# Performance work log

Hardware: AMD Instinct MI355X
Metric: run time of the kernel (lower is better)

The kernel has to match this reference:

```python
import jax, jax.numpy as jnp
import numpy as np


def setup_inputs() -> dict:
    key = jax.random.key(0)
    k1, k2, k3 = jax.random.split(key, 3)
    B, c_in, T, N = 16, 64, 64, 512
    K, c_out = 3, 64
    x = jax.random.normal(k1, (B, c_in, T, N), dtype=jnp.float32)
    # scaled Laplacian-like matrix; scale to keep Chebyshev recurrence stable
    La = jax.random.normal(k2, (B, N, N), dtype=jnp.float32) / jnp.sqrt(jnp.float32(N))
    # Conv2d(K*c_in, c_out, 1x1, bias=False) weight, squeezed to [c_out, K*c_in]
    W = jax.random.normal(k3, (c_out, K * c_in), dtype=jnp.float32) * 0.05
    return {"x": x, "La": La, "W": W}


def reference(x, La, W):
    # x: [B, c_in, T, N], La: [B, N, N], W: [c_out, K*c_in]
    B, c_in, T, N = x.shape
    K = W.shape[1] // c_in
    xp = jnp.transpose(x, (0, 1, 3, 2))  # [B, c_in, N, T] -> 'bcnl'
    # Chebyshev polynomial recurrence: T0 = I, T1 = La, Tk = 2*La@T_{k-1} - T_{k-2}
    I = jnp.broadcast_to(jnp.eye(N, dtype=x.dtype), (B, N, N))
    Ls = [I, La]
    L0, L1 = I, La
    for _ in range(2, K):
        L2 = 2.0 * jnp.matmul(La, L1) - L0
        L0, L1 = L1, L2
        Ls.append(L2)
    Lap = jnp.stack(Ls, axis=1)            # [B, K, N, N]
    Lap = jnp.swapaxes(Lap, -1, -2)        # transpose(-1,-2) as in torch
    # graph conv: contract over source node n
    y = jnp.einsum('bcnl,bknq->bckql', xp, Lap)  # [B, c_in, K, N, T]
    y = y.reshape(B, c_in * K, N, T)       # channel index = c*K + k
    # 1x1 conv, no bias: [c_out, c_in*K] x [B, c_in*K, N, T]
    out = jnp.einsum('oi,binl->bonl', W, y)  # [B, c_out, N, T]
    out = jnp.transpose(out, (0, 1, 3, 2))   # [B, c_out, T, N]
    return out
```

## Files before the change

kernel.cpp:

```cpp
#include <hip/hip_runtime.h>
#include <hip/hip_bf16.h>


#define B_   16
#define CIN  64
#define T_   64
#define N_   512
#define M_   4096
#define KDIM 512
#define COUT 64

typedef __bf16 bf16x8 __attribute__((ext_vector_type(8)));
typedef float  floatx4 __attribute__((ext_vector_type(4)));

__device__ __forceinline__ float bf2f(unsigned short u) {
    unsigned int v = ((unsigned int)u) << 16;
    return __builtin_bit_cast(float, v);
}
__device__ __forceinline__ unsigned short f2bf(float f) {
    unsigned int u = __builtin_bit_cast(unsigned int, f);
    unsigned int lsb = (u >> 16) & 1u;
    u += 0x7fffu + lsb;
    return (unsigned short)(u >> 16);
}

#define GLOAD_LDS16(gp, lp)                                                  \
    __builtin_amdgcn_global_load_lds(                                        \
        (const __attribute__((address_space(1))) void*)(gp),                 \
        (__attribute__((address_space(3))) void*)(lp), 16, 0, 0)

__global__ __launch_bounds__(256) void cvt_f32_bf16(
    const float* __restrict__ src, unsigned short* __restrict__ dst, int n)
{
    int i = (blockIdx.x * 256 + threadIdx.x) * 8;
    if (i + 8 <= n) {
        float4 a = *(const float4*)(src + i);
        float4 b = *(const float4*)(src + i + 4);
        union { unsigned short s[8]; uint4 u; } o;
        o.s[0] = f2bf(a.x); o.s[1] = f2bf(a.y); o.s[2] = f2bf(a.z); o.s[3] = f2bf(a.w);
        o.s[4] = f2bf(b.x); o.s[5] = f2bf(b.y); o.s[6] = f2bf(b.z); o.s[7] = f2bf(b.w);
        *(uint4*)(dst + i) = o.u;
    }
}

__global__ __launch_bounds__(256) void pack_w(
    const float* __restrict__ W, unsigned short* __restrict__ Wb)
{
    int idx = threadIdx.x + blockIdx.x * 256;
    if (idx < 64 * 192) {
        int o = idx / 192, j = idx % 192;
        int c = j & 63, k = j >> 6;
        Wb[idx] = f2bf(W[o * 192 + c * 3 + k]);
    }
}

#define BM 128
#define BN 128
#define BK 32

__global__ __launch_bounds__(256) void gemm_bt(
    const unsigned short* __restrict__ A,
    const unsigned short* __restrict__ Bm,
    unsigned short* __restrict__ C,
    const unsigned short* __restrict__ X,
    int mode)
{
    int batch = blockIdx.z;
    A  += (size_t)batch * M_ * KDIM;
    Bm += (size_t)batch * N_ * KDIM;
    C  += (size_t)batch * M_ * N_;
    X  += (size_t)batch * M_ * N_;
    int m0 = blockIdx.y * BM;
    int n0 = blockIdx.x * BN;

    __shared__ __align__(16) unsigned short As[BM * BK];
    __shared__ __align__(16) unsigned short Bs[BN * BK];

    int tid  = threadIdx.x;
    int lane = tid & 63;
    int wave = tid >> 6;
    int wm   = (wave >> 1) * 64;
    int wn   = (wave & 1) * 64;
    int l15  = lane & 15;
    int quad = lane >> 4;

    int r16 = lane >> 2;
    int sch = lane & 3;
    int gch = sch ^ (r16 & 3);

    const unsigned short* gA0 = A  + (size_t)(m0 + wave * 16 + r16) * KDIM + gch * 8;
    const unsigned short* gA1 = gA0 + (size_t)64 * KDIM;
    const unsigned short* gB0 = Bm + (size_t)(n0 + wave * 16 + r16) * KDIM + gch * 8;
    const unsigned short* gB1 = gB0 + (size_t)64 * KDIM;
    const unsigned short* lA0 = &As[(wave * 16) * BK];
    const unsigned short* lA1 = &As[(64 + wave * 16) * BK];
    const unsigned short* lB0 = &Bs[(wave * 16) * BK];
    const unsigned short* lB1 = &Bs[(64 + wave * 16) * BK];

    const uint4* afp[4];
    const uint4* bfp[4];
    int sl = quad ^ (l15 & 3);
#pragma unroll
    for (int im = 0; im < 4; im++)
        afp[im] = (const uint4*)((const char*)As + (wm + im * 16 + l15) * (BK * 2) + sl * 16);
#pragma unroll
    for (int jn = 0; jn < 4; jn++)
        bfp[jn] = (const uint4*)((const char*)Bs + (wn + jn * 16 + l15) * (BK * 2) + sl * 16);

    floatx4 acc[4][4];
#pragma unroll
    for (int i = 0; i < 4; i++)
#pragma unroll
        for (int j = 0; j < 4; j++) acc[i][j] = (floatx4)0.0f;

    for (int k0 = 0; k0 < KDIM; k0 += BK) {
        __syncthreads();
        GLOAD_LDS16(gA0 + k0, lA0);
        GLOAD_LDS16(gA1 + k0, lA1);
        GLOAD_LDS16(gB0 + k0, lB0);
        GLOAD_LDS16(gB1 + k0, lB1);
        __syncthreads();

        bf16x8 af[4], bf[4];
#pragma unroll
        for (int im = 0; im < 4; im++) af[im] = __builtin_bit_cast(bf16x8, *afp[im]);
#pragma unroll
        for (int jn = 0; jn < 4; jn++) bf[jn] = __builtin_bit_cast(bf16x8, *bfp[jn]);
#pragma unroll
        for (int im = 0; im < 4; im++)
#pragma unroll
            for (int jn = 0; jn < 4; jn++)
                acc[im][jn] = __builtin_amdgcn_mfma_f32_16x16x32_bf16(
                    af[im], bf[jn], acc[im][jn], 0, 0, 0);
    }

#pragma unroll
    for (int im = 0; im < 4; im++)
#pragma unroll
        for (int jn = 0; jn < 4; jn++) {
            int c = n0 + wn + jn * 16 + l15;
#pragma unroll
            for (int r = 0; r < 4; r++) {
                int m = m0 + wm + im * 16 + quad * 4 + r;
                size_t idx = (size_t)m * N_ + c;
                float v = acc[im][jn][r];
                if (mode) v = 2.0f * v - bf2f(X[idx]);
                C[idx] = f2bf(v);
            }
        }
}

#define PJ_PITCH 40

__global__ __launch_bounds__(256) void proj(
    const unsigned short* __restrict__ xb,
    const unsigned short* __restrict__ z1b,
    const unsigned short* __restrict__ z2b,
    const unsigned short* __restrict__ Wb,
    float* __restrict__ out)
{
    __shared__ __align__(16) unsigned short Ds[256 * PJ_PITCH];

    int b  = blockIdx.y;
    int n0 = blockIdx.x * 256;
    int tid  = threadIdx.x;
    int lane = tid & 63;
    int wave = tid >> 6;
    int l15  = lane & 15;
    int quad = lane >> 4;

    size_t boff = (size_t)b * M_ * N_ + n0;
    const unsigned short* zp[3] = { xb + boff, z1b + boff, z2b + boff };

    bf16x8 wf[6];
#pragma unroll
    for (int kc = 0; kc < 6; kc++)
        wf[kc] = __builtin_bit_cast(bf16x8,
            *(const uint4*)(Wb + (size_t)(wave * 16 + l15) * 192 + kc * 32 + quad * 8));

    floatx4 acc[16];
#pragma unroll
    for (int i = 0; i < 16; i++) acc[i] = (floatx4)0.0f;

    int jl  = tid & 31;
    int nc0 = (tid >> 5) * 8;

    for (int kc = 0; kc < 6; kc++) {
        const unsigned short* src =
            zp[kc >> 1] + (size_t)((kc & 1) * 32 + jl) * (T_ * N_) + nc0;
        uint4 v[4];
#pragma unroll
        for (int u = 0; u < 4; u++) v[u] = *(const uint4*)(src + u * 64);

        __syncthreads();
#pragma unroll
        for (int u = 0; u < 4; u++) {
            unsigned short* d = &Ds[(size_t)(nc0 + u * 64) * PJ_PITCH + jl];
            unsigned int w0 = v[u].x, w1 = v[u].y, w2 = v[u].z, w3 = v[u].w;
            d[0 * PJ_PITCH] = (unsigned short)w0;
            d[1 * PJ_PITCH] = (unsigned short)(w0 >> 16);
            d[2 * PJ_PITCH] = (unsigned short)w1;
            d[3 * PJ_PITCH] = (unsigned short)(w1 >> 16);
            d[4 * PJ_PITCH] = (unsigned short)w2;
            d[5 * PJ_PITCH] = (unsigned short)(w2 >> 16);
            d[6 * PJ_PITCH] = (unsigned short)w3;
            d[7 * PJ_PITCH] = (unsigned short)(w3 >> 16);
        }
        __syncthreads();

#pragma unroll
        for (int nt = 0; nt < 16; nt++) {
            bf16x8 bf = __builtin_bit_cast(bf16x8,
                *(const uint4*)(&Ds[(size_t)(nt * 16 + l15) * PJ_PITCH + quad * 8]));
            acc[nt] = __builtin_amdgcn_mfma_f32_16x16x32_bf16(wf[kc], bf, acc[nt], 0, 0, 0);
        }
    }

    float* ob = out + (size_t)b * COUT * (T_ * N_);
#pragma unroll
    for (int nt = 0; nt < 16; nt++) {
        int n = n0 + nt * 16 + l15;
#pragma unroll
        for (int r = 0; r < 4; r++) {
            int o = wave * 16 + quad * 4 + r;
            ob[(size_t)o * (T_ * N_) + n] = acc[nt][r];
        }
    }
}

extern "C" void kernel_launch(void* const* d_in, const int* in_sizes, int n_in,
                              void* d_out, int out_size, void* d_ws, size_t ws_size,
                              hipStream_t stream) {
    const float* x  = (const float*)d_in[0];
    const float* La = (const float*)d_in[1];
    const float* W  = (const float*)d_in[2];
    float* out = (float*)d_out;

    const size_t n_x  = (size_t)B_ * CIN * T_ * N_;
    const size_t n_La = (size_t)B_ * N_ * N_;

    char* ws = (char*)d_ws;
    unsigned short* xb  = (unsigned short*)ws;
    unsigned short* Lab = (unsigned short*)(ws + n_x * 2);
    unsigned short* z1b = (unsigned short*)(ws + n_x * 2 + n_La * 2);
    unsigned short* z2b = (unsigned short*)(ws + n_x * 4 + n_La * 2);
    unsigned short* Wb  = (unsigned short*)(ws + n_x * 6 + n_La * 2);

    cvt_f32_bf16<<<(int)(n_x / 2048),  256, 0, stream>>>(x,  xb,  (int)n_x);
    cvt_f32_bf16<<<(int)(n_La / 2048), 256, 0, stream>>>(La, Lab, (int)n_La);
    pack_w<<<48, 256, 0, stream>>>(W, Wb);

    dim3 gg(N_ / BN, M_ / BM, B_);
    gemm_bt<<<gg, 256, 0, stream>>>(xb,  Lab, z1b, xb, 0);
    gemm_bt<<<gg, 256, 0, stream>>>(z1b, Lab, z2b, xb, 1);

    dim3 gp((T_ * N_) / 256, B_);
    proj<<<gp, 256, 0, stream>>>(xb, z1b, z2b, Wb, out);
}
```

Baseline: 469.2 us.

## Triple-buffer GEMM LDS staging and rework projection transpose with perm-packed swizzled stores

```diff
diff --git a/kernel.cpp b/kernel.cpp
--- a/kernel.cpp
+++ b/kernel.cpp
@@ -12,6 +12,7 @@
 
 typedef __bf16 bf16x8 __attribute__((ext_vector_type(8)));
 typedef float  floatx4 __attribute__((ext_vector_type(4)));
+typedef unsigned int uintx4 __attribute__((ext_vector_type(4)));
 
 __device__ __forceinline__ float bf2f(unsigned short u) {
     unsigned int v = ((unsigned int)u) << 16;
@@ -57,6 +58,8 @@
 #define BM 128
 #define BN 128
 #define BK 32
+#define KIT  (KDIM / BK)
+#define SBUF (BM * BK)
 
 __global__ __launch_bounds__(256) void gemm_bt(
     const unsigned short* __restrict__ A,
@@ -73,8 +76,8 @@
     int m0 = blockIdx.y * BM;
     int n0 = blockIdx.x * BN;
 
-    __shared__ __align__(16) unsigned short As[BM * BK];
-    __shared__ __align__(16) unsigned short Bs[BN * BK];
+    __shared__ __align__(16) unsigned short As[3 * SBUF];
+    __shared__ __align__(16) unsigned short Bs[3 * SBUF];
 
     int tid  = threadIdx.x;
     int lane = tid & 63;
@@ -92,20 +95,27 @@
     const unsigned short* gA1 = gA0 + (size_t)64 * KDIM;
     const unsigned short* gB0 = Bm + (size_t)(n0 + wave * 16 + r16) * KDIM + gch * 8;
     const unsigned short* gB1 = gB0 + (size_t)64 * KDIM;
-    const unsigned short* lA0 = &As[(wave * 16) * BK];
-    const unsigned short* lA1 = &As[(64 + wave * 16) * BK];
-    const unsigned short* lB0 = &Bs[(wave * 16) * BK];
-    const unsigned short* lB1 = &Bs[(64 + wave * 16) * BK];
-
-    const uint4* afp[4];
-    const uint4* bfp[4];
+
+    int dA0 = (wave * 16) * BK;
+    int dA1 = (64 + wave * 16) * BK;
+    int dB0 = dA0;
+    int dB1 = dA1;
+
+#define STAGE(kk, bo) do {                                        \
+        GLOAD_LDS16(gA0 + (kk) * BK, &As[(bo) + dA0]);            \
+        GLOAD_LDS16(gA1 + (kk) * BK, &As[(bo) + dA1]);            \
+        GLOAD_LDS16(gB0 + (kk) * BK, &Bs[(bo) + dB0]);            \
+        GLOAD_LDS16(gB1 + (kk) * BK, &Bs[(bo) + dB1]);            \
+    } while (0)
+
+    int aoff[4], boff[4];
     int sl = quad ^ (l15 & 3);
 #pragma unroll
     for (int im = 0; im < 4; im++)
-        afp[im] = (const uint4*)((const char*)As + (wm + im * 16 + l15) * (BK * 2) + sl * 16);
+        aoff[im] = (wm + im * 16 + l15) * BK + sl * 8;
 #pragma unroll
     for (int jn = 0; jn < 4; jn++)
-        bfp[jn] = (const uint4*)((const char*)Bs + (wn + jn * 16 + l15) * (BK * 2) + sl * 16);
+        boff[jn] = (wn + jn * 16 + l15) * BK + sl * 8;
 
     floatx4 acc[4][4];
 #pragma unroll
@@ -113,19 +123,25 @@
 #pragma unroll
         for (int j = 0; j < 4; j++) acc[i][j] = (floatx4)0.0f;
 
-    for (int k0 = 0; k0 < KDIM; k0 += BK) {
-        __syncthreads();
-        GLOAD_LDS16(gA0 + k0, lA0);
-        GLOAD_LDS16(gA1 + k0, lA1);
-        GLOAD_LDS16(gB0 + k0, lB0);
-        GLOAD_LDS16(gB1 + k0, lB1);
-        __syncthreads();
-
+    STAGE(0, 0);
+    STAGE(1, SBUF);
+
+#pragma unroll
+    for (int k = 0; k < KIT; ++k) {
+        if (k < KIT - 1) asm volatile("s_waitcnt vmcnt(4)" ::: "memory");
+        else             asm volatile("s_waitcnt vmcnt(0)" ::: "memory");
+        __builtin_amdgcn_s_barrier();
+
+        if (k + 2 < KIT) STAGE(k + 2, ((k + 2) % 3) * SBUF);
+
+        const int cb = (k % 3) * SBUF;
         bf16x8 af[4], bf[4];
 #pragma unroll
-        for (int im = 0; im < 4; im++) af[im] = __builtin_bit_cast(bf16x8, *afp[im]);
-#pragma unroll
-        for (int jn = 0; jn < 4; jn++) bf[jn] = __builtin_bit_cast(bf16x8, *bfp[jn]);
+        for (int im = 0; im < 4; im++)
+            af[im] = __builtin_bit_cast(bf16x8, *(const uint4*)&As[cb + aoff[im]]);
+#pragma unroll
+        for (int jn = 0; jn < 4; jn++)
+            bf[jn] = __builtin_bit_cast(bf16x8, *(const uint4*)&Bs[cb + boff[jn]]);
 #pragma unroll
         for (int im = 0; im < 4; im++)
 #pragma unroll
@@ -133,6 +149,7 @@
                 acc[im][jn] = __builtin_amdgcn_mfma_f32_16x16x32_bf16(
                     af[im], bf[jn], acc[im][jn], 0, 0, 0);
     }
+#undef STAGE
 
 #pragma unroll
     for (int im = 0; im < 4; im++)
@@ -150,8 +167,6 @@
         }
 }
 
-#define PJ_PITCH 40
-
 __global__ __launch_bounds__(256) void proj(
     const unsigned short* __restrict__ xb,
     const unsigned short* __restrict__ z1b,
@@ -159,7 +174,7 @@
     const unsigned short* __restrict__ Wb,
     float* __restrict__ out)
 {
-    __shared__ __align__(16) unsigned short Ds[256 * PJ_PITCH];
+    __shared__ __align__(16) unsigned short Ds[256 * 64];
 
     int b  = blockIdx.y;
     int n0 = blockIdx.x * 256;
@@ -182,37 +197,50 @@
 #pragma unroll
     for (int i = 0; i < 16; i++) acc[i] = (floatx4)0.0f;
 
-    int jl  = tid & 31;
-    int nc0 = (tid >> 5) * 8;
-
-    for (int kc = 0; kc < 6; kc++) {
-        const unsigned short* src =
-            zp[kc >> 1] + (size_t)((kc & 1) * 32 + jl) * (T_ * N_) + nc0;
-        uint4 v[4];
-#pragma unroll
-        for (int u = 0; u < 4; u++) v[u] = *(const uint4*)(src + u * 64);
-
+    int c0  = (tid >> 5) * 8;
+    int nl0 = (tid & 31) * 8;
+    int swz = ((tid >> 5) ^ (tid & 7)) & 7;
+
+    uintx4 v[8];
+#pragma unroll
+    for (int r = 0; r < 8; r++)
+        v[r] = *(const uintx4*)(zp[0] + (size_t)(c0 + r) * (T_ * N_) + nl0);
+
+#pragma unroll
+    for (int a = 0; a < 3; a++) {
         __syncthreads();
-#pragma unroll
-        for (int u = 0; u < 4; u++) {
-            unsigned short* d = &Ds[(size_t)(nc0 + u * 64) * PJ_PITCH + jl];
-            unsigned int w0 = v[u].x, w1 = v[u].y, w2 = v[u].z, w3 = v[u].w;
-            d[0 * PJ_PITCH] = (unsigned short)w0;
-            d[1 * PJ_PITCH] = (unsigned short)(w0 >> 16);
-            d[2 * PJ_PITCH] = (unsigned short)w1;
-            d[3 * PJ_PITCH] = (unsigned short)(w1 >> 16);
-            d[4 * PJ_PITCH] = (unsigned short)w2;
-            d[5 * PJ_PITCH] = (unsigned short)(w2 >> 16);
-            d[6 * PJ_PITCH] = (unsigned short)w3;
-            d[7 * PJ_PITCH] = (unsigned short)(w3 >> 16);
+
+#pragma unroll
+        for (int i = 0; i < 8; i++) {
+            const int wi = i >> 1;
+            const unsigned sel = (i & 1) ? 0x07060302u : 0x05040100u;
+            uintx4 t;
+            t[0] = __builtin_amdgcn_perm(v[1][wi], v[0][wi], sel);
+            t[1] = __builtin_amdgcn_perm(v[3][wi], v[2][wi], sel);
+            t[2] = __builtin_amdgcn_perm(v[5][wi], v[4][wi], sel);
+            t[3] = __builtin_amdgcn_perm(v[7][wi], v[6][wi], sel);
+            *(uintx4*)&Ds[(size_t)(nl0 + i) * 64 + swz * 8] = t;
         }
         __syncthreads();
 
-#pragma unroll
-        for (int nt = 0; nt < 16; nt++) {
-            bf16x8 bf = __builtin_bit_cast(bf16x8,
-                *(const uint4*)(&Ds[(size_t)(nt * 16 + l15) * PJ_PITCH + quad * 8]));
-            acc[nt] = __builtin_amdgcn_mfma_f32_16x16x32_bf16(wf[kc], bf, acc[nt], 0, 0, 0);
+        if (a < 2) {
+#pragma unroll
+            for (int r = 0; r < 8; r++)
+                v[r] = *(const uintx4*)(zp[a + 1] + (size_t)(c0 + r) * (T_ * N_) + nl0);
+        }
+
+#pragma unroll
+        for (int ks = 0; ks < 2; ks++) {
+            const int kc = a * 2 + ks;
+#pragma unroll
+            for (int nt = 0; nt < 16; nt++) {
+                int n  = nt * 16 + l15;
+                int ch = ((ks * 4 + quad) ^ ((n >> 3) & 7)) & 7;
+                bf16x8 bfr = __builtin_bit_cast(bf16x8,
+                    *(const uint4*)&Ds[(size_t)n * 64 + ch * 8]);
+                acc[nt] = __builtin_amdgcn_mfma_f32_16x16x32_bf16(
+                    wf[kc], bfr, acc[nt], 0, 0, 0);
+            }
         }
     }
 
```

After: 441.4 us. -5.9%, faster.

## Triple-buffer GEMM LDS loads, remap blocks per XCD, adjust LDS swizzle

Applied to the files above, without the earlier changes.

```diff
diff --git a/kernel.cpp b/kernel.cpp
--- a/kernel.cpp
+++ b/kernel.cpp
@@ -57,6 +57,8 @@
 #define BM 128
 #define BN 128
 #define BK 32
+#define KIT  (KDIM / BK)
+#define SBUF (BM * BK)
 
 __global__ __launch_bounds__(256) void gemm_bt(
     const unsigned short* __restrict__ A,
@@ -65,16 +67,21 @@
     const unsigned short* __restrict__ X,
     int mode)
 {
-    int batch = blockIdx.z;
+    int h     = blockIdx.x;
+    int g     = h & 7;
+    int idx   = h >> 3;
+    int batch = g * 2 + (idx >> 7);
+    int local = idx & 127;
+    int n0    = (local & 3) * BN;
+    int m0    = (local >> 2) * BM;
+
     A  += (size_t)batch * M_ * KDIM;
     Bm += (size_t)batch * N_ * KDIM;
     C  += (size_t)batch * M_ * N_;
     X  += (size_t)batch * M_ * N_;
-    int m0 = blockIdx.y * BM;
-    int n0 = blockIdx.x * BN;
-
-    __shared__ __align__(16) unsigned short As[BM * BK];
-    __shared__ __align__(16) unsigned short Bs[BN * BK];
+
+    __shared__ __align__(16) unsigned short As[3 * SBUF];
+    __shared__ __align__(16) unsigned short Bs[3 * SBUF];
 
     int tid  = threadIdx.x;
     int lane = tid & 63;
@@ -86,26 +93,33 @@
 
     int r16 = lane >> 2;
     int sch = lane & 3;
-    int gch = sch ^ (r16 & 3);
+    int gch = sch ^ ((r16 >> 1) & 3);
 
     const unsigned short* gA0 = A  + (size_t)(m0 + wave * 16 + r16) * KDIM + gch * 8;
     const unsigned short* gA1 = gA0 + (size_t)64 * KDIM;
     const unsigned short* gB0 = Bm + (size_t)(n0 + wave * 16 + r16) * KDIM + gch * 8;
     const unsigned short* gB1 = gB0 + (size_t)64 * KDIM;
-    const unsigned short* lA0 = &As[(wave * 16) * BK];
-    const unsigned short* lA1 = &As[(64 + wave * 16) * BK];
-    const unsigned short* lB0 = &Bs[(wave * 16) * BK];
-    const unsigned short* lB1 = &Bs[(64 + wave * 16) * BK];
-
-    const uint4* afp[4];
-    const uint4* bfp[4];
-    int sl = quad ^ (l15 & 3);
+
+    int dA0 = (wave * 16) * BK;
+    int dA1 = (64 + wave * 16) * BK;
+    int dB0 = dA0;
+    int dB1 = dA1;
+
+#define STAGE(kk, bo) do {                                        \
+        GLOAD_LDS16(gA0 + (kk) * BK, &As[(bo) + dA0]);            \
+        GLOAD_LDS16(gA1 + (kk) * BK, &As[(bo) + dA1]);            \
+        GLOAD_LDS16(gB0 + (kk) * BK, &Bs[(bo) + dB0]);            \
+        GLOAD_LDS16(gB1 + (kk) * BK, &Bs[(bo) + dB1]);            \
+    } while (0)
+
+    int aoff[4], boff[4];
+    int sl = quad ^ ((l15 >> 1) & 3);
 #pragma unroll
     for (int im = 0; im < 4; im++)
-        afp[im] = (const uint4*)((const char*)As + (wm + im * 16 + l15) * (BK * 2) + sl * 16);
+        aoff[im] = (wm + im * 16 + l15) * BK + sl * 8;
 #pragma unroll
     for (int jn = 0; jn < 4; jn++)
-        bfp[jn] = (const uint4*)((const char*)Bs + (wn + jn * 16 + l15) * (BK * 2) + sl * 16);
+        boff[jn] = (wn + jn * 16 + l15) * BK + sl * 8;
 
     floatx4 acc[4][4];
 #pragma unroll
@@ -113,19 +127,25 @@
 #pragma unroll
         for (int j = 0; j < 4; j++) acc[i][j] = (floatx4)0.0f;
 
-    for (int k0 = 0; k0 < KDIM; k0 += BK) {
-        __syncthreads();
-        GLOAD_LDS16(gA0 + k0, lA0);
-        GLOAD_LDS16(gA1 + k0, lA1);
-        GLOAD_LDS16(gB0 + k0, lB0);
-        GLOAD_LDS16(gB1 + k0, lB1);
-        __syncthreads();
-
+    STAGE(0, 0);
+    STAGE(1, SBUF);
+
+#pragma unroll
+    for (int k = 0; k < KIT; ++k) {
+        if (k < KIT - 1) asm volatile("s_waitcnt vmcnt(4)" ::: "memory");
+        else             asm volatile("s_waitcnt vmcnt(0)" ::: "memory");
+        __builtin_amdgcn_s_barrier();
+
+        if (k + 2 < KIT) STAGE(k + 2, ((k + 2) % 3) * SBUF);
+
+        const int cb = (k % 3) * SBUF;
         bf16x8 af[4], bf[4];
 #pragma unroll
-        for (int im = 0; im < 4; im++) af[im] = __builtin_bit_cast(bf16x8, *afp[im]);
-#pragma unroll
-        for (int jn = 0; jn < 4; jn++) bf[jn] = __builtin_bit_cast(bf16x8, *bfp[jn]);
+        for (int im = 0; im < 4; im++)
+            af[im] = __builtin_bit_cast(bf16x8, *(const uint4*)&As[cb + aoff[im]]);
+#pragma unroll
+        for (int jn = 0; jn < 4; jn++)
+            bf[jn] = __builtin_bit_cast(bf16x8, *(const uint4*)&Bs[cb + boff[jn]]);
 #pragma unroll
         for (int im = 0; im < 4; im++)
 #pragma unroll
@@ -133,6 +153,7 @@
                 acc[im][jn] = __builtin_amdgcn_mfma_f32_16x16x32_bf16(
                     af[im], bf[jn], acc[im][jn], 0, 0, 0);
     }
+#undef STAGE
 
 #pragma unroll
     for (int im = 0; im < 4; im++)
@@ -142,10 +163,10 @@
 #pragma unroll
             for (int r = 0; r < 4; r++) {
                 int m = m0 + wm + im * 16 + quad * 4 + r;
-                size_t idx = (size_t)m * N_ + c;
+                size_t idx2 = (size_t)m * N_ + c;
                 float v = acc[im][jn][r];
-                if (mode) v = 2.0f * v - bf2f(X[idx]);
-                C[idx] = f2bf(v);
+                if (mode) v = 2.0f * v - bf2f(X[idx2]);
+                C[idx2] = f2bf(v);
             }
         }
 }
@@ -210,9 +231,9 @@
 
 #pragma unroll
         for (int nt = 0; nt < 16; nt++) {
-            bf16x8 bf = __builtin_bit_cast(bf16x8,
+            bf16x8 bfr = __builtin_bit_cast(bf16x8,
                 *(const uint4*)(&Ds[(size_t)(nt * 16 + l15) * PJ_PITCH + quad * 8]));
-            acc[nt] = __builtin_amdgcn_mfma_f32_16x16x32_bf16(wf[kc], bf, acc[nt], 0, 0, 0);
+            acc[nt] = __builtin_amdgcn_mfma_f32_16x16x32_bf16(wf[kc], bfr, acc[nt], 0, 0, 0);
         }
     }
 
@@ -250,9 +271,8 @@
     cvt_f32_bf16<<<(int)(n_La / 2048), 256, 0, stream>>>(La, Lab, (int)n_La);
     pack_w<<<48, 256, 0, stream>>>(W, Wb);
 
-    dim3 gg(N_ / BN, M_ / BM, B_);
-    gemm_bt<<<gg, 256, 0, stream>>>(xb,  Lab, z1b, xb, 0);
-    gemm_bt<<<gg, 256, 0, stream>>>(z1b, Lab, z2b, xb, 1);
+    gemm_bt<<<2048, 256, 0, stream>>>(xb,  Lab, z1b, xb, 0);
+    gemm_bt<<<2048, 256, 0, stream>>>(z1b, Lab, z2b, xb, 1);
 
     dim3 gp((T_ * N_) / 256, B_);
     proj<<<gp, 256, 0, stream>>>(xb, z1b, z2b, Wb, out);
```

New measurement: 424.7 us. -9.5%, faster.
